# Optimization experiments

Measured on AMD Instinct MI355X. Metric: run time of the kernel, lower is better.

The kernel has to match this reference:

```python
import jax, jax.numpy as jnp
import numpy as np


def setup_inputs() -> dict:
    key = jax.random.key(0)
    kx, ky = jax.random.split(key)
    B, N, M, D = 8, 4096, 4096, 128
    x = jax.random.normal(kx, (B, N, D), dtype=jnp.float32)
    y = jax.random.normal(ky, (B, M, D), dtype=jnp.float32)
    return {"x": x, "y": y}


def reference(x, y):
    # Pairwise L2 distances, equivalent to torch.cdist(x, y) (p=2).
    # ||x_i - y_j||^2 = ||x_i||^2 + ||y_j||^2 - 2 <x_i, y_j>
    x2 = jnp.sum(x * x, axis=-1)[:, :, None]          # [B, N, 1]
    y2 = jnp.sum(y * y, axis=-1)[:, None, :]          # [B, 1, M]
    xy = jnp.einsum("bnd,bmd->bnm", x, y)             # [B, N, M]
    D = jnp.sqrt(jnp.maximum(x2 + y2 - 2.0 * xy, 0.0))  # [B, N, M]
    coverage = D.min(axis=1).mean(axis=-1)            # min over N -> [B, M] -> [B]
    precision = D.min(axis=2).mean(axis=-1)           # min over M -> [B, N] -> [B]
    return (coverage + precision).mean()              # scalar Chamfer loss
```

## Files before the change

kernel.cpp:

```cpp
#include <hip/hip_runtime.h>
#include <cstdint>


#define B_   8
#define N_   4096
#define M_   4096
#define D_   128
#define TPB  8
#define ROWS_PB 512
#define XG   (N_ / ROWS_PB)
#define CHUNKS (M_ / (TPB * 128))

typedef __bf16 bf16x8 __attribute__((ext_vector_type(8)));
typedef float  f32x4  __attribute__((ext_vector_type(4)));
typedef unsigned int u32;

static __device__ __forceinline__ unsigned short f2bf(float f) {
  unsigned u = __float_as_uint(f);
  u += 0x7FFFu + ((u >> 16) & 1u);
  return (unsigned short)(u >> 16);
}

static __device__ __forceinline__ void gld16(void* lds, const void* g) {
  __builtin_amdgcn_global_load_lds(
      (const __attribute__((address_space(1))) void*)g,
      (__attribute__((address_space(3))) void*)lds, 16, 0, 0);
}

__global__ __launch_bounds__(256) void pass1_prep(
    const float* __restrict__ x, const float* __restrict__ y,
    unsigned short* __restrict__ xb, unsigned short* __restrict__ yb,
    float* __restrict__ x2, float* __restrict__ y2)
{
  const int ROWS = B_ * N_;
  int gw   = (blockIdx.x * 256 + threadIdx.x) >> 6;
  int lane = threadIdx.x & 63;
  int half = lane >> 5, sub = lane & 31;
  int row2 = gw * 2 + half;
  bool isx = row2 < ROWS;
  const float* src; unsigned short* dst; float* nrm; int row;
  if (isx) { src = x; dst = xb; nrm = x2; row = row2; }
  else     { src = y; dst = yb; nrm = y2; row = row2 - ROWS; }
  size_t base = (size_t)row * D_ + sub * 4;
  float4 v = *(const float4*)(src + base);
  float sx = isx ? -2.0f : 1.0f;
  u32 p0 = (u32)f2bf(sx * v.x) | ((u32)f2bf(sx * v.y) << 16);
  u32 p1 = (u32)f2bf(sx * v.z) | ((u32)f2bf(sx * v.w) << 16);
  *(uint2*)(dst + base) = make_uint2(p0, p1);
  float s = v.x * v.x + v.y * v.y + v.z * v.z + v.w * v.w;
  #pragma unroll
  for (int m = 1; m < 32; m <<= 1) s += __shfl_xor(s, m, 64);
  if (sub == 0) nrm[row] = s;
}

__global__
__attribute__((amdgpu_waves_per_eu(4, 4)))
__launch_bounds__(1024)
void pass2_tile(
    const unsigned short* __restrict__ xb, const unsigned short* __restrict__ yb,
    const float* __restrict__ x2, const float* __restrict__ y2,
    float* __restrict__ rowpart, float* __restrict__ colpart)
{
  __shared__ unsigned short ys[2 * 16384];
  __shared__ float cminW[2][16 * 128];
  __shared__ float y2s[TPB * 128];

  const int tid  = threadIdx.x;
  const int wave = tid >> 6;
  const int lane = tid & 63;
  const int quad = lane >> 4;
  const int l15  = lane & 15;

  const int id    = blockIdx.x;
  const int b     = id & 7;
  const int j     = id >> 3;
  const int xg    = j & 7;
  const int chunk = j >> 3;
  const int n0    = xg * ROWS_PB;
  const int mc0   = chunk * (TPB * 128);

  int srcoff[2], ldsoff[2];
  #pragma unroll
  for (int i = 0; i < 2; ++i) {
    int p  = (wave * 2 + i) * 1024 + lane * 16;
    int r  = p >> 8;
    int pc = (p >> 4) & 15;
    int c  = pc ^ (r & 15);
    srcoff[i] = r * D_ + c * 8;
    ldsoff[i] = (wave * 2 + i) * 1024;
  }

  {
    const unsigned short* src = yb + ((size_t)b * M_ + mc0) * D_;
    gld16((char*)ys + ldsoff[0], src + srcoff[0]);
    gld16((char*)ys + ldsoff[1], src + srcoff[1]);
  }
  y2s[tid] = y2[(size_t)b * M_ + mc0 + tid];

  bf16x8 afrag[4][2];
  const size_t xrow0 = (size_t)b * N_ + n0 + wave * 32;
  #pragma unroll
  for (int kb = 0; kb < 4; ++kb)
    #pragma unroll
    for (int rt = 0; rt < 2; ++rt)
      afrag[kb][rt] = *(const bf16x8*)(xb + (xrow0 + rt * 16 + l15) * D_ + kb * 32 + quad * 8);

  float xv[2][4];
  #pragma unroll
  for (int rt = 0; rt < 2; ++rt)
    #pragma unroll
    for (int r = 0; r < 4; ++r)
      xv[rt][r] = x2[(size_t)b * N_ + n0 + wave * 32 + rt * 16 + quad * 4 + r];

  const float FINF = __uint_as_float(0x7F800000u);
  float rmin2[2][4] = {{FINF, FINF, FINF, FINF}, {FINF, FINF, FINF, FINF}};

  #pragma unroll 1
  for (int t = 0; t < TPB; ++t) {
    const int m0 = mc0 + t * 128;
    const int d  = (t & 1) * 32768;
    __syncthreads();

    if (t + 1 < TPB) {
      const unsigned short* src = yb + ((size_t)b * M_ + m0 + 128) * D_;
      char* dst = (char*)ys + (32768 - d);
      gld16(dst + ldsoff[0], src + srcoff[0]);
      gld16(dst + ldsoff[1], src + srcoff[1]);
    }

    if (t > 0 && tid < 128) {
      float v = cminW[(t - 1) & 1][tid];
      #pragma unroll
      for (int w = 1; w < 16; ++w) v = fminf(v, cminW[(t - 1) & 1][w * 128 + tid]);
      colpart[(size_t)xg * (B_ * M_) + (size_t)b * M_ + (m0 - 128) + tid] = v;
    }

    #pragma unroll
    for (int ct = 0; ct < 8; ++ct) {
      f32x4 a0 = (f32x4)(0.0f), a1 = (f32x4)(0.0f);
      #pragma unroll
      for (int kb = 0; kb < 4; ++kb) {
        const int row = ct * 16 + l15;
        const int pcB = (kb * 4 + quad) ^ l15;
        bf16x8 bfr = *(const bf16x8*)((const char*)ys + d + row * 256 + pcB * 16);
        a0 = __builtin_amdgcn_mfma_f32_16x16x32_bf16(afrag[kb][0], bfr, a0, 0, 0, 0);
        a1 = __builtin_amdgcn_mfma_f32_16x16x32_bf16(afrag[kb][1], bfr, a1, 0, 0, 0);
      }
      float yv = y2s[t * 128 + ct * 16 + l15];
      float cm = FINF;
      #pragma unroll
      for (int r = 0; r < 4; ++r) {
        float s0 = a0[r] + xv[0][r] + yv;
        float s1 = a1[r] + xv[1][r] + yv;
        rmin2[0][r] = fminf(rmin2[0][r], s0);
        rmin2[1][r] = fminf(rmin2[1][r], s1);
        cm = fminf(cm, fminf(s0, s1));
      }
      cm = fminf(cm, __shfl_xor(cm, 16, 64));
      cm = fminf(cm, __shfl_xor(cm, 32, 64));
      if (lane < 16) cminW[t & 1][wave * 128 + ct * 16 + lane] = cm;
    }
  }

  __syncthreads();
  if (tid < 128) {
    float v = cminW[(TPB - 1) & 1][tid];
    #pragma unroll
    for (int w = 1; w < 16; ++w) v = fminf(v, cminW[(TPB - 1) & 1][w * 128 + tid]);
    colpart[(size_t)xg * (B_ * M_) + (size_t)b * M_ + (mc0 + (TPB - 1) * 128) + tid] = v;
  }

  #pragma unroll
  for (int rt = 0; rt < 2; ++rt) {
    #pragma unroll
    for (int r = 0; r < 4; ++r) {
      float v = rmin2[rt][r];
      v = fminf(v, __shfl_xor(v, 1, 64));
      v = fminf(v, __shfl_xor(v, 2, 64));
      v = fminf(v, __shfl_xor(v, 4, 64));
      v = fminf(v, __shfl_xor(v, 8, 64));
      if (l15 == 0)
        rowpart[(size_t)chunk * (B_ * N_) + (size_t)b * N_ + n0 + wave * 32 + rt * 16 + quad * 4 + r] = v;
    }
  }
}

__global__ __launch_bounds__(256) void pass3_partial(
    const float* __restrict__ rowpart, const float* __restrict__ colpart,
    float* __restrict__ partial)
{
  const int BN = B_ * N_;
  float s1 = 0.0f, s2 = 0.0f;
  for (int i = blockIdx.x * 256 + threadIdx.x; i < BN; i += 64 * 256) {
    float r = rowpart[i];
    #pragma unroll
    for (int c = 1; c < CHUNKS; ++c) r = fminf(r, rowpart[c * BN + i]);
    s1 += sqrtf(fmaxf(r, 0.0f));
    float m = colpart[i];
    #pragma unroll
    for (int g = 1; g < XG; ++g) m = fminf(m, colpart[g * BN + i]);
    s2 += sqrtf(fmaxf(m, 0.0f));
  }
  #pragma unroll
  for (int m = 1; m < 64; m <<= 1) { s1 += __shfl_xor(s1, m, 64); s2 += __shfl_xor(s2, m, 64); }
  __shared__ float r1[4], r2[4];
  int wave = threadIdx.x >> 6, lane = threadIdx.x & 63;
  if (lane == 0) { r1[wave] = s1; r2[wave] = s2; }
  __syncthreads();
  if (threadIdx.x == 0) {
    partial[blockIdx.x]      = r1[0] + r1[1] + r1[2] + r1[3];
    partial[64 + blockIdx.x] = r2[0] + r2[1] + r2[2] + r2[3];
  }
}

__global__ void pass4_final(const float* __restrict__ partial, float* __restrict__ out)
{
  int lane = threadIdx.x;
  float s = partial[lane] + partial[64 + lane];
  #pragma unroll
  for (int m = 1; m < 64; m <<= 1) s += __shfl_xor(s, m, 64);
  if (lane == 0) out[0] = s / (float)(B_ * N_);
}

extern "C" void kernel_launch(void* const* d_in, const int* in_sizes, int n_in,
                              void* d_out, int out_size, void* d_ws, size_t ws_size,
                              hipStream_t stream)
{
  const float* x = (const float*)d_in[0];
  const float* y = (const float*)d_in[1];
  char* ws = (char*)d_ws;

  unsigned short* xb = (unsigned short*)(ws);
  unsigned short* yb = (unsigned short*)(ws + (8u << 20));
  float* x2      = (float*)(ws + (16u << 20));
  float* y2      = (float*)(ws + (16u << 20) + (1u << 17));
  float* rowpart = (float*)(ws + (16u << 20) + (2u << 17));
  float* colpart = (float*)(ws + (16u << 20) + (6u << 17));
  float* partial = (float*)(ws + (16u << 20) + (14u << 17));
  float* outf = (float*)d_out;

  pass1_prep<<<(B_ * N_) / 4, 256, 0, stream>>>(x, y, xb, yb, x2, y2);

  pass2_tile<<<B_ * XG * CHUNKS, 1024, 0, stream>>>(xb, yb, x2, y2, rowpart, colpart);

  pass3_partial<<<64, 256, 0, stream>>>(rowpart, colpart, partial);
  pass4_final<<<1, 64, 0, stream>>>(partial, outf);
}
```

Measured before the change: 129.6 us.

## Halve waves per block and give each wave 64 query rows

Each block of pass2 now has 8 waves instead of 16, and each wave owns 64 x rows (4 row tiles) instead of 32, so every B-fragment LDS read feeds 4 MFMAs rather than 2. This cuts LDS read traffic per MFMA and halves the cross-wave column-min reduction. The cost is more registers per thread for fragments and accumulators, and fewer waves per block to hide latency. The Y tile load is redistributed across the smaller block.

```diff
diff --git a/kernel.cpp b/kernel.cpp
--- a/kernel.cpp
+++ b/kernel.cpp
@@ -54,15 +54,15 @@
 }
 
 __global__
-__attribute__((amdgpu_waves_per_eu(4, 4)))
-__launch_bounds__(1024)
+__launch_bounds__(512)
+__attribute__((amdgpu_waves_per_eu(2)))
 void pass2_tile(
     const unsigned short* __restrict__ xb, const unsigned short* __restrict__ yb,
     const float* __restrict__ x2, const float* __restrict__ y2,
     float* __restrict__ rowpart, float* __restrict__ colpart)
 {
   __shared__ unsigned short ys[2 * 16384];
-  __shared__ float cminW[2][16 * 128];
+  __shared__ float cminW[2][8 * 128];
   __shared__ float y2s[TPB * 128];
 
   const int tid  = threadIdx.x;
@@ -79,41 +79,41 @@
   const int n0    = xg * ROWS_PB;
   const int mc0   = chunk * (TPB * 128);
 
-  int srcoff[2], ldsoff[2];
-  #pragma unroll
-  for (int i = 0; i < 2; ++i) {
-    int p  = (wave * 2 + i) * 1024 + lane * 16;
-    int r  = p >> 8;
-    int pc = (p >> 4) & 15;
-    int c  = pc ^ (r & 15);
-    srcoff[i] = r * D_ + c * 8;
-    ldsoff[i] = (wave * 2 + i) * 1024;
-  }
-
   {
     const unsigned short* src = yb + ((size_t)b * M_ + mc0) * D_;
-    gld16((char*)ys + ldsoff[0], src + srcoff[0]);
-    gld16((char*)ys + ldsoff[1], src + srcoff[1]);
-  }
-  y2s[tid] = y2[(size_t)b * M_ + mc0 + tid];
-
-  bf16x8 afrag[4][2];
-  const size_t xrow0 = (size_t)b * N_ + n0 + wave * 32;
+    #pragma unroll
+    for (int i = 0; i < 4; ++i) {
+      int p  = (wave * 4 + i) * 1024 + lane * 16;
+      int r  = p >> 8;
+      int pc = (p >> 4) & 15;
+      int c  = pc ^ (r & 15);
+      gld16((char*)ys + (wave * 4 + i) * 1024, src + r * D_ + c * 8);
+    }
+  }
+  y2s[tid]       = y2[(size_t)b * M_ + mc0 + tid];
+  y2s[tid + 512] = y2[(size_t)b * M_ + mc0 + tid + 512];
+
+  bf16x8 afrag[4][4];
+  const size_t xrow0 = (size_t)b * N_ + n0 + wave * 64;
   #pragma unroll
   for (int kb = 0; kb < 4; ++kb)
     #pragma unroll
-    for (int rt = 0; rt < 2; ++rt)
+    for (int rt = 0; rt < 4; ++rt)
       afrag[kb][rt] = *(const bf16x8*)(xb + (xrow0 + rt * 16 + l15) * D_ + kb * 32 + quad * 8);
 
-  float xv[2][4];
-  #pragma unroll
-  for (int rt = 0; rt < 2; ++rt)
+  float xv[4][4];
+  #pragma unroll
+  for (int rt = 0; rt < 4; ++rt)
     #pragma unroll
     for (int r = 0; r < 4; ++r)
-      xv[rt][r] = x2[(size_t)b * N_ + n0 + wave * 32 + rt * 16 + quad * 4 + r];
+      xv[rt][r] = x2[(size_t)b * N_ + n0 + wave * 64 + rt * 16 + quad * 4 + r];
 
   const float FINF = __uint_as_float(0x7F800000u);
-  float rmin2[2][4] = {{FINF, FINF, FINF, FINF}, {FINF, FINF, FINF, FINF}};
+  float rmin2[4][4];
+  #pragma unroll
+  for (int rt = 0; rt < 4; ++rt)
+    #pragma unroll
+    for (int r = 0; r < 4; ++r) rmin2[rt][r] = FINF;
 
   #pragma unroll 1
   for (int t = 0; t < TPB; ++t) {
@@ -124,37 +124,47 @@
     if (t + 1 < TPB) {
       const unsigned short* src = yb + ((size_t)b * M_ + m0 + 128) * D_;
       char* dst = (char*)ys + (32768 - d);
-      gld16(dst + ldsoff[0], src + srcoff[0]);
-      gld16(dst + ldsoff[1], src + srcoff[1]);
+      #pragma unroll
+      for (int i = 0; i < 4; ++i) {
+        int p  = (wave * 4 + i) * 1024 + lane * 16;
+        int r  = p >> 8;
+        int pc = (p >> 4) & 15;
+        int c  = pc ^ (r & 15);
+        gld16(dst + (wave * 4 + i) * 1024, src + r * D_ + c * 8);
+      }
     }
 
     if (t > 0 && tid < 128) {
       float v = cminW[(t - 1) & 1][tid];
       #pragma unroll
-      for (int w = 1; w < 16; ++w) v = fminf(v, cminW[(t - 1) & 1][w * 128 + tid]);
+      for (int w = 1; w < 8; ++w) v = fminf(v, cminW[(t - 1) & 1][w * 128 + tid]);
       colpart[(size_t)xg * (B_ * M_) + (size_t)b * M_ + (m0 - 128) + tid] = v;
     }
 
     #pragma unroll
     for (int ct = 0; ct < 8; ++ct) {
-      f32x4 a0 = (f32x4)(0.0f), a1 = (f32x4)(0.0f);
+      f32x4 a[4];
+      #pragma unroll
+      for (int rt = 0; rt < 4; ++rt) a[rt] = (f32x4)(0.0f);
       #pragma unroll
       for (int kb = 0; kb < 4; ++kb) {
         const int row = ct * 16 + l15;
         const int pcB = (kb * 4 + quad) ^ l15;
         bf16x8 bfr = *(const bf16x8*)((const char*)ys + d + row * 256 + pcB * 16);
-        a0 = __builtin_amdgcn_mfma_f32_16x16x32_bf16(afrag[kb][0], bfr, a0, 0, 0, 0);
-        a1 = __builtin_amdgcn_mfma_f32_16x16x32_bf16(afrag[kb][1], bfr, a1, 0, 0, 0);
+        #pragma unroll
+        for (int rt = 0; rt < 4; ++rt)
+          a[rt] = __builtin_amdgcn_mfma_f32_16x16x32_bf16(afrag[kb][rt], bfr, a[rt], 0, 0, 0);
       }
       float yv = y2s[t * 128 + ct * 16 + l15];
       float cm = FINF;
       #pragma unroll
-      for (int r = 0; r < 4; ++r) {
-        float s0 = a0[r] + xv[0][r] + yv;
-        float s1 = a1[r] + xv[1][r] + yv;
-        rmin2[0][r] = fminf(rmin2[0][r], s0);
-        rmin2[1][r] = fminf(rmin2[1][r], s1);
-        cm = fminf(cm, fminf(s0, s1));
+      for (int rt = 0; rt < 4; ++rt) {
+        #pragma unroll
+        for (int r = 0; r < 4; ++r) {
+          float s = a[rt][r] + xv[rt][r] + yv;
+          rmin2[rt][r] = fminf(rmin2[rt][r], s);
+          cm = fminf(cm, s);
+        }
       }
       cm = fminf(cm, __shfl_xor(cm, 16, 64));
       cm = fminf(cm, __shfl_xor(cm, 32, 64));
@@ -166,12 +176,12 @@
   if (tid < 128) {
     float v = cminW[(TPB - 1) & 1][tid];
     #pragma unroll
-    for (int w = 1; w < 16; ++w) v = fminf(v, cminW[(TPB - 1) & 1][w * 128 + tid]);
+    for (int w = 1; w < 8; ++w) v = fminf(v, cminW[(TPB - 1) & 1][w * 128 + tid]);
     colpart[(size_t)xg * (B_ * M_) + (size_t)b * M_ + (mc0 + (TPB - 1) * 128) + tid] = v;
   }
 
   #pragma unroll
-  for (int rt = 0; rt < 2; ++rt) {
+  for (int rt = 0; rt < 4; ++rt) {
     #pragma unroll
     for (int r = 0; r < 4; ++r) {
       float v = rmin2[rt][r];
@@ -180,7 +190,7 @@
       v = fminf(v, __shfl_xor(v, 4, 64));
       v = fminf(v, __shfl_xor(v, 8, 64));
       if (l15 == 0)
-        rowpart[(size_t)chunk * (B_ * N_) + (size_t)b * N_ + n0 + wave * 32 + rt * 16 + quad * 4 + r] = v;
+        rowpart[(size_t)chunk * (B_ * N_) + (size_t)b * N_ + n0 + wave * 64 + rt * 16 + quad * 4 + r] = v;
     }
   }
 }
@@ -241,7 +251,7 @@
 
   pass1_prep<<<(B_ * N_) / 4, 256, 0, stream>>>(x, y, xb, yb, x2, y2);
 
-  pass2_tile<<<B_ * XG * CHUNKS, 1024, 0, stream>>>(xb, yb, x2, y2, rowpart, colpart);
+  pass2_tile<<<B_ * XG * CHUNKS, 512, 0, stream>>>(xb, yb, x2, y2, rowpart, colpart);
 
   pass3_partial<<<64, 256, 0, stream>>>(rowpart, colpart, partial);
   pass4_final<<<1, 64, 0, stream>>>(partial, outf);
```

Measured after the change: 122.1 us. -5.7%, faster.
